# Kernel tuning notes

Hardware: AMD Instinct MI355X
Metric: run time of the kernel (lower is better)

Reference implementation:

```python
import jax, jax.numpy as jnp
import numpy as np

V, E, C = 50000, 5000, 16
TAU = 0.5
EPS = 1e-08
SPARSITY = 0.02  # fraction of (v,e) incidences


def setup_inputs() -> dict:
    key = jax.random.key(0)
    k1, k2, k3, k4 = jax.random.split(key, 4)
    pred_s = jax.random.normal(k1, (V, C), dtype=jnp.float32)
    pred_t = jax.random.normal(k2, (V, C), dtype=jnp.float32)
    # binary incidence matrix; pin vertex 0 into every edge so deg_e > 0
    H = (jax.random.uniform(k3, (V, E)) < SPARSITY).astype(jnp.float32)
    H = H.at[0, :].set(1.0)
    e_mask = jax.random.randint(k4, (E,), 0, 2).astype(jnp.bool_)
    return {"pred_s": pred_s, "pred_t": pred_t, "H": H, "e_mask": e_mask}


def _v2e_mean(p, H, deg_e):
    # == einsum('vc,ve->ec', p, H @ diag(1/deg_e)) : column-normalized scatter-mean
    return jnp.einsum('ve,vc->ec', H, p) / deg_e[:, None]


def reference(pred_s, pred_t, H, e_mask):
    ps = jax.nn.softmax(pred_s, axis=1)   # [V, C]
    pt = jax.nn.softmax(pred_t, axis=1)   # [V, C]
    deg_e = H.sum(axis=0)                 # [E]
    log_s = jnp.log(_v2e_mean(ps, H, deg_e) / TAU + EPS)  # [E, C]
    log_t = jnp.log(_v2e_mean(pt, H, deg_e) / TAU + EPS)  # [E, C]
    # F.kl_div(input=log_s, target=log_t, log_target=True, reduction='batchmean')
    # restricted to masked edges; mask via weights to keep shapes static.
    kl = jnp.exp(log_t) * (log_t - log_s)                  # [E, C]
    m = e_mask.astype(kl.dtype)                            # [E]
    n_sel = jnp.maximum(m.sum(), 1.0)
    return (kl * m[:, None]).sum() / n_sel
```

## Files before the change

### kernel.cpp

```cpp
#include <hip/hip_runtime.h>

#define NV 50000
#define NE 5000
#define NC 16
#define TAU_INV 2.0f
#define EPS 1e-8f

#define NCH 100
#define VCH 500
#define GRP 4
#define EPL 2
#define NXB 10
#define NBLK (NXB * NCH)
#define NLANE 5120

typedef float vf4 __attribute__((ext_vector_type(4)));
typedef float vf2 __attribute__((ext_vector_type(2)));

__global__ __launch_bounds__(256) void softmax_kernel(
    const float* __restrict__ pred_s, const float* __restrict__ pred_t,
    float* __restrict__ p) {
  int i = blockIdx.x * 256 + threadIdx.x;
  if (i >= 2 * NV) return;
  const float* src;
  float* dst;
  if (i < NV) { src = pred_s + (size_t)i * NC; dst = p + (size_t)i * 32; }
  else        { int j = i - NV; src = pred_t + (size_t)j * NC; dst = p + (size_t)j * 32 + 16; }
  float4 a = ((const float4*)src)[0];
  float4 b = ((const float4*)src)[1];
  float4 c = ((const float4*)src)[2];
  float4 d = ((const float4*)src)[3];
  float x[16] = {a.x,a.y,a.z,a.w, b.x,b.y,b.z,b.w, c.x,c.y,c.z,c.w, d.x,d.y,d.z,d.w};
  float mx = x[0];
#pragma unroll
  for (int k = 1; k < 16; ++k) mx = fmaxf(mx, x[k]);
  float sum = 0.f;
#pragma unroll
  for (int k = 0; k < 16; ++k) { x[k] = expf(x[k] - mx); sum += x[k]; }
  float inv = 1.f / sum;
#pragma unroll
  for (int k = 0; k < 16; ++k) x[k] *= inv;
  float4 o0 = {x[0], x[1], x[2], x[3]};
  float4 o1 = {x[4], x[5], x[6], x[7]};
  float4 o2 = {x[8], x[9], x[10], x[11]};
  float4 o3 = {x[12], x[13], x[14], x[15]};
  ((float4*)dst)[0] = o0;
  ((float4*)dst)[1] = o1;
  ((float4*)dst)[2] = o2;
  ((float4*)dst)[3] = o3;
}

#define Q4(ACC, B) \
  ACC[B+0].x = fmaf(h.x, q.x, ACC[B+0].x); ACC[B+0].y = fmaf(h.y, q.x, ACC[B+0].y); \
  ACC[B+1].x = fmaf(h.x, q.y, ACC[B+1].x); ACC[B+1].y = fmaf(h.y, q.y, ACC[B+1].y); \
  ACC[B+2].x = fmaf(h.x, q.z, ACC[B+2].x); ACC[B+2].y = fmaf(h.y, q.z, ACC[B+2].y); \
  ACC[B+3].x = fmaf(h.x, q.w, ACC[B+3].x); ACC[B+3].y = fmaf(h.y, q.w, ACC[B+3].y);

__global__ __launch_bounds__(256, 4) void accum_kernel(
    const float* __restrict__ H, const float* __restrict__ p,
    float* __restrict__ part) {
  int b = blockIdx.x;
  int item = (b & 7) * 125 + (b >> 3);
  int xb = item % NXB;
  int y  = item / NXB;
  int e0 = EPL * (xb * 256 + (int)threadIdx.x);
  if (e0 > NE - EPL) e0 = NE - EPL;
  int v0 = y * VCH;

  float2 aS[16], aT[16];
#pragma unroll
  for (int k = 0; k < 16; ++k) {
    aS[k] = make_float2(0.f, 0.f);
    aT[k] = make_float2(0.f, 0.f);
  }
  float2 dg = make_float2(0.f, 0.f);

  const float* __restrict__ hp = H + (size_t)v0 * NE + e0;
  const float4* __restrict__ pr = (const float4*)(p + (size_t)v0 * 32);

  vf2 hc[GRP];
#pragma unroll
  for (int u = 0; u < GRP; ++u)
    hc[u] = *(const vf2*)(hp + (size_t)u * NE);

  for (int vb = 0; vb < VCH; vb += GRP) {
    int nb = (vb + GRP < VCH) ? vb + GRP : vb;
    vf2 hn[GRP];
#pragma unroll
    for (int u = 0; u < GRP; ++u)
      hn[u] = *(const vf2*)(hp + (size_t)(nb + u) * NE);

#pragma unroll
    for (int u = 0; u < GRP; ++u) {
      const float4* __restrict__ r = pr + (size_t)(vb + u) * 8;
      vf2 h = hc[u];
      dg.x += h.x; dg.y += h.y;
      float4 q;
      q = r[0]; Q4(aS, 0)
      q = r[1]; Q4(aS, 4)
      q = r[2]; Q4(aS, 8)
      q = r[3]; Q4(aS, 12)
      q = r[4]; Q4(aT, 0)
      q = r[5]; Q4(aT, 4)
      q = r[6]; Q4(aT, 8)
      q = r[7]; Q4(aT, 12)
    }
#pragma unroll
    for (int u = 0; u < GRP; ++u) hc[u] = hn[u];
  }

  float* op = part + (size_t)y * 33 * NLANE + e0;
#pragma unroll
  for (int k = 0; k < 16; ++k) {
    vf2 w = {aS[k].x, aS[k].y};
    *(vf2*)(op + (size_t)k * NLANE) = w;
  }
#pragma unroll
  for (int k = 0; k < 16; ++k) {
    vf2 w = {aT[k].x, aT[k].y};
    *(vf2*)(op + (size_t)(16 + k) * NLANE) = w;
  }
  {
    vf2 w = {dg.x, dg.y};
    *(vf2*)(op + (size_t)32 * NLANE) = w;
  }
}

__global__ __launch_bounds__(256) void reduce_kernel(
    const float* __restrict__ part, float* __restrict__ acc) {
  int i = blockIdx.x * 256 + threadIdx.x;
  if (i >= 33 * NLANE) return;
  float s = 0.f;
#pragma unroll 4
  for (int y = 0; y < NCH; ++y)
    s += part[(size_t)y * 33 * NLANE + i];
  acc[i] = s;
}

__global__ __launch_bounds__(256) void kl_kernel(
    const float* __restrict__ acc, const unsigned char* __restrict__ e_mask,
    float* __restrict__ out) {
  __shared__ float snum[4];
  __shared__ float scnt[4];
  int t = threadIdx.x;
  float num = 0.f, cnt = 0.f;
  for (int e = t; e < NE; e += 256) {
    if (e_mask[e]) {
      float deg = acc[(size_t)32 * NLANE + e];
      float invd = 1.f / deg;
      float kl = 0.f;
#pragma unroll
      for (int k = 0; k < 16; ++k) {
        float ms = acc[(size_t)k * NLANE + e] * invd;
        float mt = acc[(size_t)(16 + k) * NLANE + e] * invd;
        float xs = ms * TAU_INV + EPS;
        float xt = mt * TAU_INV + EPS;
        kl += xt * (logf(xt) - logf(xs));
      }
      num += kl;
      cnt += 1.f;
    }
  }
#pragma unroll
  for (int off = 32; off > 0; off >>= 1) {
    num += __shfl_down(num, off, 64);
    cnt += __shfl_down(cnt, off, 64);
  }
  if ((t & 63) == 0) { snum[t >> 6] = num; scnt[t >> 6] = cnt; }
  __syncthreads();
  if (t == 0) {
    float n = snum[0] + snum[1] + snum[2] + snum[3];
    float c2 = scnt[0] + scnt[1] + scnt[2] + scnt[3];
    out[0] = n / fmaxf(c2, 1.f);
  }
}

extern "C" void kernel_launch(void* const* d_in, const int* in_sizes, int n_in,
                              void* d_out, int out_size, void* d_ws, size_t ws_size,
                              hipStream_t stream) {
  const float* pred_s = (const float*)d_in[0];
  const float* pred_t = (const float*)d_in[1];
  const float* H      = (const float*)d_in[2];
  const unsigned char* e_mask = (const unsigned char*)d_in[3];

  float* ws   = (float*)d_ws;
  float* p    = ws;
  float* acc  = ws + (size_t)NV * 32;
  float* part = acc + (size_t)33 * NLANE;

  softmax_kernel<<<dim3((2 * NV + 255) / 256), 256, 0, stream>>>(pred_s, pred_t, p);
  accum_kernel<<<dim3(NBLK), 256, 0, stream>>>(H, p, part);
  reduce_kernel<<<dim3((33 * NLANE + 255) / 256), 256, 0, stream>>>(part, acc);
  kl_kernel<<<1, 256, 0, stream>>>(acc, e_mask, (float*)d_out);
}
```

Baseline: 1.432 ms.

## Replace dense H-times-p accumulation with scan-to-sparse lists plus gather

The dense FMA pass over the whole incidence matrix is replaced by two kernels. A scan kernel streams H once with nontemporal loads and records, for each edge and each 100-vertex sub-chunk, the local indices of nonzero vertices in fixed-capacity ushort lists with counts. A gather kernel stages the chunk's softmax rows in swizzled LDS and sums only the listed rows per edge, cutting the dense FLOPs down to the nonzeros. The trade-off is extra workspace, scattered list writes, a fixed per-list capacity of 64 that could overflow on denser inputs, and data-dependent loop lengths.

```diff
diff --git a/kernel.cpp b/kernel.cpp
--- a/kernel.cpp
+++ b/kernel.cpp
@@ -8,10 +8,12 @@
 
 #define NCH 100
 #define VCH 500
-#define GRP 4
+#define NSUB 5
+#define SUBV 100
+#define CAP 64
+#define NEP 5120
 #define EPL 2
 #define NXB 10
-#define NBLK (NXB * NCH)
 #define NLANE 5120
 
 typedef float vf4 __attribute__((ext_vector_type(4)));
@@ -50,15 +52,53 @@
   ((float4*)dst)[3] = o3;
 }
 
-#define Q4(ACC, B) \
-  ACC[B+0].x = fmaf(h.x, q.x, ACC[B+0].x); ACC[B+0].y = fmaf(h.y, q.x, ACC[B+0].y); \
-  ACC[B+1].x = fmaf(h.x, q.y, ACC[B+1].x); ACC[B+1].y = fmaf(h.y, q.y, ACC[B+1].y); \
-  ACC[B+2].x = fmaf(h.x, q.z, ACC[B+2].x); ACC[B+2].y = fmaf(h.y, q.z, ACC[B+2].y); \
-  ACC[B+3].x = fmaf(h.x, q.w, ACC[B+3].x); ACC[B+3].y = fmaf(h.y, q.w, ACC[B+3].y);
-
-__global__ __launch_bounds__(256, 4) void accum_kernel(
-    const float* __restrict__ H, const float* __restrict__ p,
-    float* __restrict__ part) {
+__global__ __launch_bounds__(256) void scan_kernel(
+    const float* __restrict__ H, unsigned short* __restrict__ lists,
+    unsigned int* __restrict__ cnt) {
+  int b = blockIdx.x;
+  int y = b / NSUB, q = b - y * NSUB;
+  int v0 = y * VCH + q * SUBV;
+  int t = threadIdx.x;
+  bool last = (t < 1250 - 1024);
+
+  unsigned int cs[5][4];
+#pragma unroll
+  for (int s = 0; s < 5; ++s)
+#pragma unroll
+    for (int c = 0; c < 4; ++c) cs[s][c] = 0;
+
+  size_t listBase = (size_t)b * CAP * NEP;
+
+  for (int r = 0; r < SUBV; ++r) {
+    const float* __restrict__ row = H + (size_t)(v0 + r) * NE;
+    unsigned short vl = (unsigned short)(q * SUBV + r);
+#pragma unroll
+    for (int s = 0; s < 5; ++s) {
+      if (s < 4 || last) {
+        int idx = s * 256 + t;
+        vf4 x = __builtin_nontemporal_load((const vf4*)(row + (size_t)idx * 4));
+        int e = idx * 4;
+        if (x.x != 0.f) { lists[listBase + (size_t)cs[s][0] * NEP + e + 0] = vl; cs[s][0]++; }
+        if (x.y != 0.f) { lists[listBase + (size_t)cs[s][1] * NEP + e + 1] = vl; cs[s][1]++; }
+        if (x.z != 0.f) { lists[listBase + (size_t)cs[s][2] * NEP + e + 2] = vl; cs[s][2]++; }
+        if (x.w != 0.f) { lists[listBase + (size_t)cs[s][3] * NEP + e + 3] = vl; cs[s][3]++; }
+      }
+    }
+  }
+#pragma unroll
+  for (int s = 0; s < 5; ++s) {
+    if (s < 4 || last) {
+      int idx = s * 256 + t;
+      uint4 w = {cs[s][0], cs[s][1], cs[s][2], cs[s][3]};
+      *(uint4*)(cnt + (size_t)b * NEP + (size_t)idx * 4) = w;
+    }
+  }
+}
+
+__global__ __launch_bounds__(256) void gather_kernel(
+    const unsigned short* __restrict__ lists, const unsigned int* __restrict__ cnt,
+    const float* __restrict__ p, float* __restrict__ part) {
+  __shared__ float lp[VCH * 32];
   int b = blockIdx.x;
   int item = (b & 7) * 125 + (b >> 3);
   int xb = item % NXB;
@@ -67,63 +107,57 @@
   if (e0 > NE - EPL) e0 = NE - EPL;
   int v0 = y * VCH;
 
-  float2 aS[16], aT[16];
+  {
+    const float* __restrict__ src = p + (size_t)v0 * 32;
+    for (int i = threadIdx.x; i < VCH * 32; i += 256) {
+      int v = i >> 5, c = i & 31;
+      lp[(v << 5) + (c ^ (v & 31))] = src[i];
+    }
+  }
+  __syncthreads();
+
+  float aS0[16], aT0[16], aS1[16], aT1[16];
+#pragma unroll
+  for (int k = 0; k < 16; ++k) { aS0[k] = 0.f; aT0[k] = 0.f; aS1[k] = 0.f; aT1[k] = 0.f; }
+  float deg0 = 0.f, deg1 = 0.f;
+
+#define EDGE_ACC(AS, AT, DEG, K)                                          \
+  {                                                                       \
+    int e = e0 + K;                                                       \
+    for (int q = 0; q < NSUB; ++q) {                                      \
+      int sb = y * NSUB + q;                                              \
+      unsigned int c = cnt[(size_t)sb * NEP + e];                         \
+      DEG += (float)c;                                                    \
+      const unsigned short* __restrict__ lb =                             \
+          lists + (size_t)sb * CAP * NEP + e;                             \
+      for (unsigned int j = 0; j < c; ++j) {                              \
+        int v = (int)lb[(size_t)j * NEP];                                 \
+        int sw = v & 31;                                                  \
+        const float* __restrict__ rp = lp + (v << 5);                     \
+        _Pragma("unroll")                                                 \
+        for (int cc = 0; cc < 16; ++cc) AS[cc] += rp[cc ^ sw];            \
+        _Pragma("unroll")                                                 \
+        for (int cc = 0; cc < 16; ++cc) AT[cc] += rp[(16 + cc) ^ sw];     \
+      }                                                                   \
+    }                                                                     \
+  }
+
+  EDGE_ACC(aS0, aT0, deg0, 0)
+  EDGE_ACC(aS1, aT1, deg1, 1)
+#undef EDGE_ACC
+
+  float* op = part + (size_t)y * 33 * NLANE + e0;
 #pragma unroll
   for (int k = 0; k < 16; ++k) {
-    aS[k] = make_float2(0.f, 0.f);
-    aT[k] = make_float2(0.f, 0.f);
-  }
-  float2 dg = make_float2(0.f, 0.f);
-
-  const float* __restrict__ hp = H + (size_t)v0 * NE + e0;
-  const float4* __restrict__ pr = (const float4*)(p + (size_t)v0 * 32);
-
-  vf2 hc[GRP];
-#pragma unroll
-  for (int u = 0; u < GRP; ++u)
-    hc[u] = *(const vf2*)(hp + (size_t)u * NE);
-
-  for (int vb = 0; vb < VCH; vb += GRP) {
-    int nb = (vb + GRP < VCH) ? vb + GRP : vb;
-    vf2 hn[GRP];
-#pragma unroll
-    for (int u = 0; u < GRP; ++u)
-      hn[u] = *(const vf2*)(hp + (size_t)(nb + u) * NE);
-
-#pragma unroll
-    for (int u = 0; u < GRP; ++u) {
-      const float4* __restrict__ r = pr + (size_t)(vb + u) * 8;
-      vf2 h = hc[u];
-      dg.x += h.x; dg.y += h.y;
-      float4 q;
-      q = r[0]; Q4(aS, 0)
-      q = r[1]; Q4(aS, 4)
-      q = r[2]; Q4(aS, 8)
-      q = r[3]; Q4(aS, 12)
-      q = r[4]; Q4(aT, 0)
-      q = r[5]; Q4(aT, 4)
-      q = r[6]; Q4(aT, 8)
-      q = r[7]; Q4(aT, 12)
-    }
-#pragma unroll
-    for (int u = 0; u < GRP; ++u) hc[u] = hn[u];
-  }
-
-  float* op = part + (size_t)y * 33 * NLANE + e0;
+    vf2 w = {aS0[k], aS1[k]};
+    *(vf2*)(op + (size_t)k * NLANE) = w;
+  }
 #pragma unroll
   for (int k = 0; k < 16; ++k) {
-    vf2 w = {aS[k].x, aS[k].y};
-    *(vf2*)(op + (size_t)k * NLANE) = w;
-  }
-#pragma unroll
-  for (int k = 0; k < 16; ++k) {
-    vf2 w = {aT[k].x, aT[k].y};
+    vf2 w = {aT0[k], aT1[k]};
     *(vf2*)(op + (size_t)(16 + k) * NLANE) = w;
   }
-  {
-    vf2 w = {dg.x, dg.y};
-    *(vf2*)(op + (size_t)32 * NLANE) = w;
-  }
+  { vf2 w = {deg0, deg1}; *(vf2*)(op + (size_t)32 * NLANE) = w; }
 }
 
 __global__ __launch_bounds__(256) void reduce_kernel(
@@ -185,11 +219,14 @@
 
   float* ws   = (float*)d_ws;
   float* p    = ws;
-  float* acc  = ws + (size_t)NV * 32;
+  float* acc  = p + (size_t)NV * 32;
   float* part = acc + (size_t)33 * NLANE;
+  unsigned int* cnt = (unsigned int*)(part + (size_t)NCH * 33 * NLANE);
+  unsigned short* lists = (unsigned short*)(cnt + (size_t)NCH * NSUB * NEP);
 
   softmax_kernel<<<dim3((2 * NV + 255) / 256), 256, 0, stream>>>(pred_s, pred_t, p);
-  accum_kernel<<<dim3(NBLK), 256, 0, stream>>>(H, p, part);
+  scan_kernel<<<dim3(NCH * NSUB), 256, 0, stream>>>(H, lists, cnt);
+  gather_kernel<<<dim3(NCH * NXB), 256, 0, stream>>>(lists, cnt, p, part);
   reduce_kernel<<<dim3((33 * NLANE + 255) / 256), 256, 0, stream>>>(part, acc);
   kl_kernel<<<1, 256, 0, stream>>>(acc, e_mask, (float*)d_out);
 }
```

Result: slower. 1.595 ms (+11.4%).
